# Performance work log

Hardware: AMD Instinct MI355X
Metric: run time of the kernel (lower is better)

## Reference

```python
import jax, jax.numpy as jnp
import numpy as np

SIZES = [128] * 16 + [64, 32, 16, 8, 4, 2, 1]
IN_SIZES = [16] + SIZES[:-1]
OFFSETS = np.concatenate([[0], np.cumsum(SIZES)])  # node offsets into packed params
TOTAL_NODES = int(OFFSETS[-1])  # 2175
N_CELLS = 262144  # 512x512 grid of cells

# Each of the 16 soft boolean gates g(a,b) is a polynomial c0 + c1*a + c2*b + c3*a*b.
# Rows ordered: FALSE, AND, A&~B, A, ~A&B, B, XOR, OR, NOR, XNOR, ~B, A|~B, ~A, ~A|B, NAND, TRUE
GATE_COEFFS = jnp.array([
    [0, 0, 0, 0], [0, 0, 0, 1], [0, 1, 0, -1], [0, 1, 0, 0],
    [0, 0, 1, -1], [0, 0, 1, 0], [0, 1, 1, -2], [0, 1, 1, -1],
    [1, -1, -1, 1], [1, -1, -1, 2], [1, 0, -1, 0], [1, 0, -1, 1],
    [1, -1, 0, 0], [1, -1, 0, 1], [1, 0, 0, -1], [1, 0, 0, 0],
], dtype=jnp.float32)


def setup_inputs() -> dict:
    key = jax.random.key(0)
    kx, kw, *kidx = jax.random.split(key, 2 + 2 * len(SIZES))
    x = jax.random.uniform(kx, (N_CELLS, IN_SIZES[0]), dtype=jnp.float32)
    W = jax.random.normal(kw, (TOTAL_NODES, 16), dtype=jnp.float32)
    ia_parts, ib_parts = [], []
    for li, (n, fan_in) in enumerate(zip(SIZES, IN_SIZES)):
        ia_parts.append(jax.random.randint(kidx[2 * li], (n,), 0, fan_in, dtype=jnp.int32))
        ib_parts.append(jax.random.randint(kidx[2 * li + 1], (n,), 0, fan_in, dtype=jnp.int32))
    idx_a = jnp.concatenate(ia_parts)
    idx_b = jnp.concatenate(ib_parts)
    return {"x": x, "W": W, "idx_a": idx_a, "idx_b": idx_b}


def _logic_layer(x, w, ia, ib, temperature):
    # x: [N, in], w: [n, 16], ia/ib: [n]
    p = jax.nn.softmax(w / temperature, axis=-1)       # [n, 16]
    c = p @ GATE_COEFFS                                # [n, 4]
    a = x[:, ia]                                       # [N, n]
    b = x[:, ib]                                       # [N, n]
    return c[:, 0] + c[:, 1] * a + c[:, 2] * b + c[:, 3] * (a * b)


def reference(x, W, idx_a, idx_b):
    temperature = 1.0
    h = x
    for li, n in enumerate(SIZES):
        s, e = int(OFFSETS[li]), int(OFFSETS[li + 1])
        h = _logic_layer(h, W[s:e], idx_a[s:e], idx_b[s:e], temperature)
    return h  # [N, 1]
```

## Files before the change

### kernel.cpp

```cpp
#include <hip/hip_runtime.h>
#include <hip/hip_fp16.h>
#include <hip/hip_bf16.h>


#define N_CELLS     262144
#define TOTAL_NODES 2175
#define CELLS       256
#define BLOCK       1024
#define ROWS        128

__device__ const float GC[16][4] = {
    {0, 0, 0, 0}, {0, 0, 0, 1}, {0, 1, 0, -1}, {0, 1, 0, 0},
    {0, 0, 1, -1}, {0, 0, 1, 0}, {0, 1, 1, -2}, {0, 1, 1, -1},
    {1, -1, -1, 1}, {1, -1, -1, 2}, {1, 0, -1, 0}, {1, 0, -1, 1},
    {1, -1, 0, 0}, {1, -1, 0, 1}, {1, 0, 0, -1}, {1, 0, 0, 0}
};

struct __align__(32) NodeDesc {
    unsigned int c0, c1, c2, c3;
    int ia, ib;
    int pad0, pad1;
};

__device__ __forceinline__ unsigned int h2u(__half2 h) {
    return *reinterpret_cast<unsigned int*>(&h);
}
__device__ __forceinline__ __half2 u2h2(unsigned int u) {
    return *reinterpret_cast<__half2*>(&u);
}

__global__ void coeff_kernel(const float* __restrict__ W,
                             const int* __restrict__ idx_a,
                             const int* __restrict__ idx_b,
                             NodeDesc* __restrict__ dout) {
    int node = blockIdx.x * blockDim.x + threadIdx.x;
    if (node >= TOTAL_NODES) return;
    const float* w = W + node * 16;
    float v[16];
    float m = -1e30f;
    #pragma unroll
    for (int i = 0; i < 16; ++i) { v[i] = w[i]; m = fmaxf(m, v[i]); }
    float s = 0.f;
    #pragma unroll
    for (int i = 0; i < 16; ++i) { v[i] = expf(v[i] - m); s += v[i]; }
    float inv = 1.0f / s;
    float c0 = 0.f, c1 = 0.f, c2 = 0.f, c3 = 0.f;
    #pragma unroll
    for (int i = 0; i < 16; ++i) {
        float p = v[i] * inv;
        c0 += p * GC[i][0];
        c1 += p * GC[i][1];
        c2 += p * GC[i][2];
        c3 += p * GC[i][3];
    }
    NodeDesc d;
    d.c0 = h2u(__half2half2(__float2half(c0)));
    d.c1 = h2u(__half2half2(__float2half(c1)));
    d.c2 = h2u(__half2half2(__float2half(c2)));
    d.c3 = h2u(__half2half2(__float2half(c3)));
    d.ia = idx_a[node]; d.ib = idx_b[node];
    d.pad0 = 0; d.pad1 = 0;
    dout[node] = d;
}

template<int PER>
__device__ __forceinline__ void layer_step(const NodeDesc* __restrict__ desc,
                                           int off, int w,
                                           uint2 (* __restrict__ buf)[64],
                                           int q, int lane) {
    const int n0 = q * PER;
    uint2 res[PER];
    const bool active = (n0 < w);

    if (active) {
        #pragma unroll
        for (int j = 0; j < PER; ++j) {
            int nu = __builtin_amdgcn_readfirstlane(n0 + j);
            NodeDesc d = desc[off + nu];
            __half2 c0 = u2h2(d.c0), c1 = u2h2(d.c1);
            __half2 c2 = u2h2(d.c2), c3 = u2h2(d.c3);
            uint2 ap = buf[d.ia][lane];
            uint2 bp = buf[d.ib][lane];
            __half2 a0 = u2h2(ap.x), a1 = u2h2(ap.y);
            __half2 b0 = u2h2(bp.x), b1 = u2h2(bp.y);
            __half2 r0 = __hfma2(a0, __hfma2(c3, b0, c1), __hfma2(c2, b0, c0));
            __half2 r1 = __hfma2(a1, __hfma2(c3, b1, c1), __hfma2(c2, b1, c0));
            res[j].x = h2u(r0);
            res[j].y = h2u(r1);
        }
    }
    __syncthreads();
    if (active) {
        #pragma unroll
        for (int j = 0; j < PER; ++j) {
            int nu = __builtin_amdgcn_readfirstlane(n0 + j);
            buf[nu][lane] = res[j];
        }
    }
    __syncthreads();
}

__global__ __launch_bounds__(BLOCK, 4)
void net_kernel(const float* __restrict__ x,
                const NodeDesc* __restrict__ desc,
                float* __restrict__ out) {
    __shared__ uint2 buf[ROWS][64];

    const int t    = threadIdx.x;
    const int lane = t & 63;
    const int q    = t >> 6;
    const size_t base = (size_t)blockIdx.x * CELLS;

    {
        const float4* xv = reinterpret_cast<const float4*>(x + base * 16);
        __half* hp = reinterpret_cast<__half*>(&buf[0][0]);
        float4 v = xv[t];
        int c  = t >> 2;
        int k  = (t & 3) << 2;
        int h  = c >> 6;
        int cl = c & 63;
        hp[((k + 0) * 64 + cl) * 4 + h] = __float2half(v.x);
        hp[((k + 1) * 64 + cl) * 4 + h] = __float2half(v.y);
        hp[((k + 2) * 64 + cl) * 4 + h] = __float2half(v.z);
        hp[((k + 3) * 64 + cl) * 4 + h] = __float2half(v.w);
    }
    __syncthreads();

    #pragma unroll 1
    for (int li = 0; li < 16; ++li)
        layer_step<8>(desc, li * 128, 128, buf, q, lane);
    layer_step<4>(desc, 2048, 64, buf, q, lane);
    layer_step<2>(desc, 2112, 32, buf, q, lane);
    layer_step<1>(desc, 2144, 16, buf, q, lane);
    layer_step<1>(desc, 2160,  8, buf, q, lane);
    layer_step<1>(desc, 2168,  4, buf, q, lane);
    layer_step<1>(desc, 2172,  2, buf, q, lane);
    layer_step<1>(desc, 2174,  1, buf, q, lane);

    if (t < CELLS) {
        int cl = t & 63, h = t >> 6;
        uint2 p = buf[0][cl];
        unsigned int u = (h < 2) ? p.x : p.y;
        __half2 hh = u2h2(u);
        out[base + t] = (h & 1) ? __high2float(hh) : __low2float(hh);
    }
}

extern "C" void kernel_launch(void* const* d_in, const int* in_sizes, int n_in,
                              void* d_out, int out_size, void* d_ws, size_t ws_size,
                              hipStream_t stream) {
    const float* x  = (const float*)d_in[0];
    const float* W  = (const float*)d_in[1];
    const int*   ia = (const int*)d_in[2];
    const int*   ib = (const int*)d_in[3];
    NodeDesc* desc  = (NodeDesc*)d_ws;

    coeff_kernel<<<(TOTAL_NODES + 255) / 256, 256, 0, stream>>>(W, ia, ib, desc);

    const int grid = N_CELLS / CELLS;
    net_kernel<<<grid, BLOCK, 0, stream>>>(x, desc, (float*)d_out);
}
```

Baseline: 136.2 us.

## Pair nodes per wave with half-wave split and 128-bit LDS accesses

Each wave now handles pairs of nodes: the low 32 lanes compute one node and the high 32 lanes the other. Each lane covers 8 cells through uint4 LDS loads and stores, so a wave makes half as many passes per layer and each LDS instruction moves 16 bytes instead of 8. The coeff kernel writes pair-packed descriptors with byte offsets precomputed, and duplicates the last layer's single node to fill the second half of the pair. In exchange the descriptor indexing and LDS layout get more complex, and the wider accesses may cause more LDS bank conflicts.

```diff
diff --git a/kernel.cpp b/kernel.cpp
--- a/kernel.cpp
+++ b/kernel.cpp
@@ -5,9 +5,19 @@
 
 #define N_CELLS     262144
 #define TOTAL_NODES 2175
+#define TOTAL_PAIRS 1088
 #define CELLS       256
 #define BLOCK       1024
 #define ROWS        128
+
+__device__ const int LAYER_OFF[24] = {
+    0, 128, 256, 384, 512, 640, 768, 896, 1024, 1152, 1280, 1408,
+    1536, 1664, 1792, 1920, 2048, 2112, 2144, 2160, 2168, 2172, 2174, 2175
+};
+__device__ const int PAIR_OFF[24] = {
+    0, 64, 128, 192, 256, 320, 384, 448, 512, 576, 640, 704,
+    768, 832, 896, 960, 1024, 1056, 1072, 1080, 1084, 1086, 1087, 1088
+};
 
 __device__ const float GC[16][4] = {
     {0, 0, 0, 0}, {0, 0, 0, 1}, {0, 1, 0, -1}, {0, 1, 0, 0},
@@ -16,11 +26,6 @@
     {1, -1, 0, 0}, {1, -1, 0, 1}, {1, 0, 0, -1}, {1, 0, 0, 0}
 };
 
-struct __align__(32) NodeDesc {
-    unsigned int c0, c1, c2, c3;
-    int ia, ib;
-    int pad0, pad1;
-};
 
 __device__ __forceinline__ unsigned int h2u(__half2 h) {
     return *reinterpret_cast<unsigned int*>(&h);
@@ -32,7 +37,7 @@
 __global__ void coeff_kernel(const float* __restrict__ W,
                              const int* __restrict__ idx_a,
                              const int* __restrict__ idx_b,
-                             NodeDesc* __restrict__ dout) {
+                             unsigned int* __restrict__ pdesc) {
     int node = blockIdx.x * blockDim.x + threadIdx.x;
     if (node >= TOTAL_NODES) return;
     const float* w = W + node * 16;
@@ -53,48 +58,63 @@
         c2 += p * GC[i][2];
         c3 += p * GC[i][3];
     }
-    NodeDesc d;
-    d.c0 = h2u(__half2half2(__float2half(c0)));
-    d.c1 = h2u(__half2half2(__float2half(c1)));
-    d.c2 = h2u(__half2half2(__float2half(c2)));
-    d.c3 = h2u(__half2half2(__float2half(c3)));
-    d.ia = idx_a[node]; d.ib = idx_b[node];
-    d.pad0 = 0; d.pad1 = 0;
-    dout[node] = d;
+    int li = 0;
+    #pragma unroll
+    for (int l = 0; l < 23; ++l) if (node >= LAYER_OFF[l + 1]) li = l + 1;
+    int nu = node - LAYER_OFF[li];
+    int p  = PAIR_OFF[li] + (nu >> 1);
+    int h  = nu & 1;
+
+    unsigned int cc0 = h2u(__half2half2(__float2half(c0)));
+    unsigned int cc1 = h2u(__half2half2(__float2half(c1)));
+    unsigned int cc2 = h2u(__half2half2(__float2half(c2)));
+    unsigned int cc3 = h2u(__half2half2(__float2half(c3)));
+    unsigned int iao = (unsigned int)idx_a[node] * 512u;
+    unsigned int ibo = (unsigned int)idx_b[node] * 512u;
+    unsigned int oo  = (unsigned int)nu * 512u;
+
+    int reps = (li == 22) ? 2 : 1;
+    for (int r = 0; r < reps; ++r) {
+        unsigned int* d = pdesc + p * 16 + (h + r) * 8;
+        d[0] = cc0; d[1] = cc1; d[2] = cc2; d[3] = cc3;
+        d[4] = iao; d[5] = ibo; d[6] = oo;  d[7] = 0;
+    }
 }
 
-template<int PER>
-__device__ __forceinline__ void layer_step(const NodeDesc* __restrict__ desc,
-                                           int off, int w,
-                                           uint2 (* __restrict__ buf)[64],
-                                           int q, int lane) {
-    const int n0 = q * PER;
-    uint2 res[PER];
-    const bool active = (n0 < w);
+template<int PP>
+__device__ __forceinline__ void layer_step(const unsigned int* __restrict__ pdesc,
+                                           int poff, int npairs,
+                                           char* __restrict__ lds,
+                                           int q, int hi32, int slot16) {
+    const int p0 = q * PP;
+    uint4 res[PP];
+    unsigned int oo[PP];
+    const bool active = (p0 < npairs);
 
     if (active) {
         #pragma unroll
-        for (int j = 0; j < PER; ++j) {
-            int nu = __builtin_amdgcn_readfirstlane(n0 + j);
-            NodeDesc d = desc[off + nu];
-            __half2 c0 = u2h2(d.c0), c1 = u2h2(d.c1);
-            __half2 c2 = u2h2(d.c2), c3 = u2h2(d.c3);
-            uint2 ap = buf[d.ia][lane];
-            uint2 bp = buf[d.ib][lane];
-            __half2 a0 = u2h2(ap.x), a1 = u2h2(ap.y);
-            __half2 b0 = u2h2(bp.x), b1 = u2h2(bp.y);
-            __half2 r0 = __hfma2(a0, __hfma2(c3, b0, c1), __hfma2(c2, b0, c0));
-            __half2 r1 = __hfma2(a1, __hfma2(c3, b1, c1), __hfma2(c2, b1, c0));
-            res[j].x = h2u(r0);
-            res[j].y = h2u(r1);
+        for (int m = 0; m < PP; ++m) {
+            int pu = __builtin_amdgcn_readfirstlane(p0 + m) + poff;
+            const unsigned int* pd = pdesc + pu * 16 + hi32;
+            uint4 cf = *reinterpret_cast<const uint4*>(pd);
+            uint4 mo = *reinterpret_cast<const uint4*>(pd + 4);
+            uint4 av = *reinterpret_cast<const uint4*>(lds + mo.x + slot16);
+            uint4 bv = *reinterpret_cast<const uint4*>(lds + mo.y + slot16);
+            __half2 C0 = u2h2(cf.x), C1 = u2h2(cf.y), C2 = u2h2(cf.z), C3 = u2h2(cf.w);
+            __half2 a0 = u2h2(av.x), a1 = u2h2(av.y), a2 = u2h2(av.z), a3 = u2h2(av.w);
+            __half2 b0 = u2h2(bv.x), b1 = u2h2(bv.y), b2 = u2h2(bv.z), b3 = u2h2(bv.w);
+            res[m].x = h2u(__hfma2(a0, __hfma2(C3, b0, C1), __hfma2(C2, b0, C0)));
+            res[m].y = h2u(__hfma2(a1, __hfma2(C3, b1, C1), __hfma2(C2, b1, C0)));
+            res[m].z = h2u(__hfma2(a2, __hfma2(C3, b2, C1), __hfma2(C2, b2, C0)));
+            res[m].w = h2u(__hfma2(a3, __hfma2(C3, b3, C1), __hfma2(C2, b3, C0)));
+            oo[m] = mo.z;
         }
     }
     __syncthreads();
     if (active) {
         #pragma unroll
-        for (int j = 0; j < PER; ++j) {
-            int nu = __builtin_amdgcn_readfirstlane(n0 + j);
-            buf[nu][lane] = res[j];
+        for (int m = 0; m < PP; ++m) {
+            *reinterpret_cast<uint4*>(lds + oo[m] + slot16) = res[m];
         }
     }
     __syncthreads();
@@ -102,47 +122,46 @@
 
 __global__ __launch_bounds__(BLOCK, 4)
 void net_kernel(const float* __restrict__ x,
-                const NodeDesc* __restrict__ desc,
+                const unsigned int* __restrict__ pdesc,
                 float* __restrict__ out) {
-    __shared__ uint2 buf[ROWS][64];
+    __shared__ uint4 buf[ROWS][32];
 
-    const int t    = threadIdx.x;
-    const int lane = t & 63;
-    const int q    = t >> 6;
+    const int t      = threadIdx.x;
+    const int lane   = t & 63;
+    const int q      = t >> 6;
+    const int hi32   = (lane >> 5) * 8;
+    const int slot16 = (lane & 31) * 16;
+    char* lds = reinterpret_cast<char*>(&buf[0][0]);
     const size_t base = (size_t)blockIdx.x * CELLS;
 
     {
         const float4* xv = reinterpret_cast<const float4*>(x + base * 16);
-        __half* hp = reinterpret_cast<__half*>(&buf[0][0]);
+        __half* hp = reinterpret_cast<__half*>(lds);
         float4 v = xv[t];
         int c  = t >> 2;
         int k  = (t & 3) << 2;
-        int h  = c >> 6;
-        int cl = c & 63;
-        hp[((k + 0) * 64 + cl) * 4 + h] = __float2half(v.x);
-        hp[((k + 1) * 64 + cl) * 4 + h] = __float2half(v.y);
-        hp[((k + 2) * 64 + cl) * 4 + h] = __float2half(v.z);
-        hp[((k + 3) * 64 + cl) * 4 + h] = __float2half(v.w);
+        int idx = (c >> 3) * 8 + (c & 7);
+        hp[(k + 0) * 256 + idx] = __float2half(v.x);
+        hp[(k + 1) * 256 + idx] = __float2half(v.y);
+        hp[(k + 2) * 256 + idx] = __float2half(v.z);
+        hp[(k + 3) * 256 + idx] = __float2half(v.w);
     }
     __syncthreads();
 
     #pragma unroll 1
     for (int li = 0; li < 16; ++li)
-        layer_step<8>(desc, li * 128, 128, buf, q, lane);
-    layer_step<4>(desc, 2048, 64, buf, q, lane);
-    layer_step<2>(desc, 2112, 32, buf, q, lane);
-    layer_step<1>(desc, 2144, 16, buf, q, lane);
-    layer_step<1>(desc, 2160,  8, buf, q, lane);
-    layer_step<1>(desc, 2168,  4, buf, q, lane);
-    layer_step<1>(desc, 2172,  2, buf, q, lane);
-    layer_step<1>(desc, 2174,  1, buf, q, lane);
+        layer_step<4>(pdesc, li * 64, 64, lds, q, hi32, slot16);
+    layer_step<2>(pdesc, 1024, 32, lds, q, hi32, slot16);
+    layer_step<1>(pdesc, 1056, 16, lds, q, hi32, slot16);
+    layer_step<1>(pdesc, 1072,  8, lds, q, hi32, slot16);
+    layer_step<1>(pdesc, 1080,  4, lds, q, hi32, slot16);
+    layer_step<1>(pdesc, 1084,  2, lds, q, hi32, slot16);
+    layer_step<1>(pdesc, 1086,  1, lds, q, hi32, slot16);
+    layer_step<1>(pdesc, 1087,  1, lds, q, hi32, slot16);
 
     if (t < CELLS) {
-        int cl = t & 63, h = t >> 6;
-        uint2 p = buf[0][cl];
-        unsigned int u = (h < 2) ? p.x : p.y;
-        __half2 hh = u2h2(u);
-        out[base + t] = (h & 1) ? __high2float(hh) : __low2float(hh);
+        const __half* hp = reinterpret_cast<const __half*>(lds);
+        out[base + t] = __half2float(hp[t]);
     }
 }
 
@@ -153,10 +172,10 @@
     const float* W  = (const float*)d_in[1];
     const int*   ia = (const int*)d_in[2];
     const int*   ib = (const int*)d_in[3];
-    NodeDesc* desc  = (NodeDesc*)d_ws;
+    unsigned int* pdesc = (unsigned int*)d_ws;
 
-    coeff_kernel<<<(TOTAL_NODES + 255) / 256, 256, 0, stream>>>(W, ia, ib, desc);
+    coeff_kernel<<<(TOTAL_NODES + 255) / 256, 256, 0, stream>>>(W, ia, ib, pdesc);
 
     const int grid = N_CELLS / CELLS;
-    net_kernel<<<grid, BLOCK, 0, stream>>>(x, desc, (float*)d_out);
+    net_kernel<<<grid, BLOCK, 0, stream>>>(x, pdesc, (float*)d_out);
 }
```

Measured after the change: 151.7 us. 1.11x slower.

## Fuse pairs of logic layers into single steps to halve barriers

Applied to the files above, without the earlier changes.

Each pair of consecutive layers is collapsed into one step. Every output node of the second layer directly evaluates its two input gates from the earlier layer, reading four shared-memory values. This cuts the number of __syncthreads rounds and shared-memory writebacks roughly in half. The cost is recomputing the first-layer gates, since a node used by several outputs is evaluated more than once, plus more descriptor loads per node. The final odd layer is handled with an identity gate.

```diff
diff --git a/kernel.cpp b/kernel.cpp
--- a/kernel.cpp
+++ b/kernel.cpp
@@ -5,9 +5,15 @@
 
 #define N_CELLS     262144
 #define TOTAL_NODES 2175
+#define TOTAL_FUSED 1067
 #define CELLS       256
 #define BLOCK       1024
 #define ROWS        128
+
+__device__ const int LAYER_OFF[24] = {
+    0, 128, 256, 384, 512, 640, 768, 896, 1024, 1152, 1280, 1408,
+    1536, 1664, 1792, 1920, 2048, 2112, 2144, 2160, 2168, 2172, 2174, 2175
+};
 
 __device__ const float GC[16][4] = {
     {0, 0, 0, 0}, {0, 0, 0, 1}, {0, 1, 0, -1}, {0, 1, 0, 0},
@@ -16,12 +22,6 @@
     {1, -1, 0, 0}, {1, -1, 0, 1}, {1, 0, 0, -1}, {1, 0, 0, 0}
 };
 
-struct __align__(32) NodeDesc {
-    unsigned int c0, c1, c2, c3;
-    int ia, ib;
-    int pad0, pad1;
-};
-
 __device__ __forceinline__ unsigned int h2u(__half2 h) {
     return *reinterpret_cast<unsigned int*>(&h);
 }
@@ -29,13 +29,7 @@
     return *reinterpret_cast<__half2*>(&u);
 }
 
-__global__ void coeff_kernel(const float* __restrict__ W,
-                             const int* __restrict__ idx_a,
-                             const int* __restrict__ idx_b,
-                             NodeDesc* __restrict__ dout) {
-    int node = blockIdx.x * blockDim.x + threadIdx.x;
-    if (node >= TOTAL_NODES) return;
-    const float* w = W + node * 16;
+__device__ __forceinline__ void softgc(const float* __restrict__ w, float* c) {
     float v[16];
     float m = -1e30f;
     #pragma unroll
@@ -44,27 +38,72 @@
     #pragma unroll
     for (int i = 0; i < 16; ++i) { v[i] = expf(v[i] - m); s += v[i]; }
     float inv = 1.0f / s;
-    float c0 = 0.f, c1 = 0.f, c2 = 0.f, c3 = 0.f;
+    c[0] = c[1] = c[2] = c[3] = 0.f;
     #pragma unroll
     for (int i = 0; i < 16; ++i) {
         float p = v[i] * inv;
-        c0 += p * GC[i][0];
-        c1 += p * GC[i][1];
-        c2 += p * GC[i][2];
-        c3 += p * GC[i][3];
-    }
-    NodeDesc d;
-    d.c0 = h2u(__half2half2(__float2half(c0)));
-    d.c1 = h2u(__half2half2(__float2half(c1)));
-    d.c2 = h2u(__half2half2(__float2half(c2)));
-    d.c3 = h2u(__half2half2(__float2half(c3)));
-    d.ia = idx_a[node]; d.ib = idx_b[node];
-    d.pad0 = 0; d.pad1 = 0;
-    dout[node] = d;
+        c[0] += p * GC[i][0];
+        c[1] += p * GC[i][1];
+        c[2] += p * GC[i][2];
+        c[3] += p * GC[i][3];
+    }
+}
+
+__device__ __forceinline__ uint4 packc(const float* c) {
+    uint4 r;
+    r.x = h2u(__half2half2(__float2half(c[0])));
+    r.y = h2u(__half2half2(__float2half(c[1])));
+    r.z = h2u(__half2half2(__float2half(c[2])));
+    r.w = h2u(__half2half2(__float2half(c[3])));
+    return r;
+}
+
+__global__ void coeff_kernel(const float* __restrict__ W,
+                             const int* __restrict__ idx_a,
+                             const int* __restrict__ idx_b,
+                             uint4* __restrict__ fdesc) {
+    int f = blockIdx.x * blockDim.x + threadIdx.x;
+    if (f >= TOTAL_FUSED) return;
+
+    int L1, n;
+    bool ident = false;
+    if (f < 1024)      { int p = f >> 7; L1 = 2 * p + 1; n = f & 127; }
+    else if (f < 1056) { L1 = 17; n = f - 1024; }
+    else if (f < 1064) { L1 = 19; n = f - 1056; }
+    else if (f < 1066) { L1 = 21; n = f - 1064; }
+    else               { L1 = 22; n = 0; ident = true; }
+
+    int g1 = LAYER_OFF[L1] + n;
+    float cO[4], cA[4], cB[4];
+    softgc(W + 16 * g1, cO);
+    uint4 idx;
+    if (!ident) {
+        int L0 = L1 - 1;
+        int gA = LAYER_OFF[L0] + idx_a[g1];
+        int gB = LAYER_OFF[L0] + idx_b[g1];
+        softgc(W + 16 * gA, cA);
+        softgc(W + 16 * gB, cB);
+        idx.x = idx_a[gA]; idx.y = idx_b[gA];
+        idx.z = idx_a[gB]; idx.w = idx_b[gB];
+    } else {
+        cA[0] = 0.f; cA[1] = 1.f; cA[2] = 0.f; cA[3] = 0.f;
+        cB[0] = 0.f; cB[1] = 1.f; cB[2] = 0.f; cB[3] = 0.f;
+        idx.x = idx.y = idx_a[g1];
+        idx.z = idx.w = idx_b[g1];
+    }
+    fdesc[f * 4 + 0] = packc(cA);
+    fdesc[f * 4 + 1] = packc(cB);
+    fdesc[f * 4 + 2] = packc(cO);
+    fdesc[f * 4 + 3] = idx;
+}
+
+__device__ __forceinline__ __half2 gate2(__half2 a, __half2 b, uint4 c) {
+    return __hfma2(a, __hfma2(u2h2(c.w), b, u2h2(c.y)),
+                      __hfma2(u2h2(c.z), b, u2h2(c.x)));
 }
 
 template<int PER>
-__device__ __forceinline__ void layer_step(const NodeDesc* __restrict__ desc,
+__device__ __forceinline__ void fused_step(const uint4* __restrict__ fdesc,
                                            int off, int w,
                                            uint2 (* __restrict__ buf)[64],
                                            int q, int lane) {
@@ -76,17 +115,20 @@
         #pragma unroll
         for (int j = 0; j < PER; ++j) {
             int nu = __builtin_amdgcn_readfirstlane(n0 + j);
-            NodeDesc d = desc[off + nu];
-            __half2 c0 = u2h2(d.c0), c1 = u2h2(d.c1);
-            __half2 c2 = u2h2(d.c2), c3 = u2h2(d.c3);
-            uint2 ap = buf[d.ia][lane];
-            uint2 bp = buf[d.ib][lane];
-            __half2 a0 = u2h2(ap.x), a1 = u2h2(ap.y);
-            __half2 b0 = u2h2(bp.x), b1 = u2h2(bp.y);
-            __half2 r0 = __hfma2(a0, __hfma2(c3, b0, c1), __hfma2(c2, b0, c0));
-            __half2 r1 = __hfma2(a1, __hfma2(c3, b1, c1), __hfma2(c2, b1, c0));
-            res[j].x = h2u(r0);
-            res[j].y = h2u(r1);
+            const uint4* fd = fdesc + 4 * (off + nu);
+            uint4 cAc = fd[0], cBc = fd[1], cOc = fd[2], idx = fd[3];
+            uint2 vaA = buf[idx.x][lane];
+            uint2 vbA = buf[idx.y][lane];
+            uint2 vaB = buf[idx.z][lane];
+            uint2 vbB = buf[idx.w][lane];
+            __half2 A0 = gate2(u2h2(vaA.x), u2h2(vbA.x), cAc);
+            __half2 A1 = gate2(u2h2(vaA.y), u2h2(vbA.y), cAc);
+            __half2 B0 = gate2(u2h2(vaB.x), u2h2(vbB.x), cBc);
+            __half2 B1 = gate2(u2h2(vaB.y), u2h2(vbB.y), cBc);
+            __half2 O0 = gate2(A0, B0, cOc);
+            __half2 O1 = gate2(A1, B1, cOc);
+            res[j].x = h2u(O0);
+            res[j].y = h2u(O1);
         }
     }
     __syncthreads();
@@ -102,7 +144,7 @@
 
 __global__ __launch_bounds__(BLOCK, 4)
 void net_kernel(const float* __restrict__ x,
-                const NodeDesc* __restrict__ desc,
+                const uint4* __restrict__ fdesc,
                 float* __restrict__ out) {
     __shared__ uint2 buf[ROWS][64];
 
@@ -127,15 +169,12 @@
     __syncthreads();
 
     #pragma unroll 1
-    for (int li = 0; li < 16; ++li)
-        layer_step<8>(desc, li * 128, 128, buf, q, lane);
-    layer_step<4>(desc, 2048, 64, buf, q, lane);
-    layer_step<2>(desc, 2112, 32, buf, q, lane);
-    layer_step<1>(desc, 2144, 16, buf, q, lane);
-    layer_step<1>(desc, 2160,  8, buf, q, lane);
-    layer_step<1>(desc, 2168,  4, buf, q, lane);
-    layer_step<1>(desc, 2172,  2, buf, q, lane);
-    layer_step<1>(desc, 2174,  1, buf, q, lane);
+    for (int p = 0; p < 8; ++p)
+        fused_step<8>(fdesc, p * 128, 128, buf, q, lane);
+    fused_step<2>(fdesc, 1024, 32, buf, q, lane);
+    fused_step<1>(fdesc, 1056,  8, buf, q, lane);
+    fused_step<1>(fdesc, 1064,  2, buf, q, lane);
+    fused_step<1>(fdesc, 1066,  1, buf, q, lane);
 
     if (t < CELLS) {
         int cl = t & 63, h = t >> 6;
@@ -153,10 +192,10 @@
     const float* W  = (const float*)d_in[1];
     const int*   ia = (const int*)d_in[2];
     const int*   ib = (const int*)d_in[3];
-    NodeDesc* desc  = (NodeDesc*)d_ws;
-
-    coeff_kernel<<<(TOTAL_NODES + 255) / 256, 256, 0, stream>>>(W, ia, ib, desc);
+    uint4* fdesc    = (uint4*)d_ws;
+
+    coeff_kernel<<<(TOTAL_FUSED + 255) / 256, 256, 0, stream>>>(W, ia, ib, fdesc);
 
     const int grid = N_CELLS / CELLS;
-    net_kernel<<<grid, BLOCK, 0, stream>>>(x, desc, (float*)d_out);
-}
+    net_kernel<<<grid, BLOCK, 0, stream>>>(x, fdesc, (float*)d_out);
+}
```

Measured after the change: 137.1 us. No clear change (+0.7%).
